# Kernel optimization log

Hardware: AMD Instinct MI355X
Metric: run time of the kernel (lower is better)

## Reference

```python
import jax, jax.numpy as jnp
import numpy as np

B, N, L, S = 32, 100000, 12, 256
SIGMA = 1.0          # gaussian filter sigma (pixels)
PIXEL = 1.0          # sampling rate (A/px)
LAMBDA = 0.0197      # electron wavelength at 300 kV (A)
CS = 2.7e7           # spherical aberration (A)
Q0 = 0.1             # amplitude contrast


def setup_inputs() -> dict:
    key = jax.random.key(0)
    ks = jax.random.split(key, 10)
    return {
        "c_nma": jax.random.normal(ks[0], (B, L), jnp.float32),
        "delta_euler": 0.1 * jax.random.normal(ks[1], (B, 3), jnp.float32),
        "delta_shifts": jax.random.normal(ks[2], (B, 2), jnp.float32),
        "coords": (jax.random.uniform(ks[3], (N, 3), jnp.float32) - 0.5) * (S / 2.0),
        "basis_x": 0.01 * jax.random.normal(ks[4], (N, L), jnp.float32),
        "basis_y": 0.01 * jax.random.normal(ks[5], (N, L), jnp.float32),
        "basis_z": 0.01 * jax.random.normal(ks[6], (N, L), jnp.float32),
        "euler_base": 2.0 * np.pi * jax.random.uniform(ks[7], (B, 3), jnp.float32),
        "shifts_base": 2.0 * jax.random.normal(ks[8], (B, 2), jnp.float32),
        "defocus": 1e4 + 1.5e4 * jax.random.uniform(ks[9], (B,), jnp.float32),
    }


def _euler_to_rot(eu):
    # ZYZ (xmipp) convention: rot, tilt, psi -> [B,3,3]
    rot, tilt, psi = eu[..., 0], eu[..., 1], eu[..., 2]
    ca, sa = jnp.cos(rot), jnp.sin(rot)
    cb, sb = jnp.cos(tilt), jnp.sin(tilt)
    cg, sg = jnp.cos(psi), jnp.sin(psi)
    r0 = jnp.stack([cg * cb * ca - sg * sa, cg * cb * sa + sg * ca, -cg * sb], -1)
    r1 = jnp.stack([-sg * cb * ca - cg * sa, -sg * cb * sa + cg * ca, sg * sb], -1)
    r2 = jnp.stack([sb * ca, sb * sa, cb], -1)
    return jnp.stack([r0, r1, r2], -2)


def _forward(c_nma, delta_euler, delta_shifts, coords, basis_x, basis_y, basis_z,
             euler_base, shifts_base, defocus):
    # deformation field + apply: [B,N]
    c_x = coords[:, 0][None, :] + jnp.einsum('bl,nl->bn', c_nma, basis_x)
    c_y = coords[:, 1][None, :] + jnp.einsum('bl,nl->bn', c_nma, basis_y)
    c_z = coords[:, 2][None, :] + jnp.einsum('bl,nl->bn', c_nma, basis_z)
    p = jnp.stack([c_x, c_y, c_z], -1)               # [B,N,3]

    # bond lengths between consecutive atoms: [B,N-1]
    dvec = p[:, 1:] - p[:, :-1]
    bondk = jnp.sqrt(jnp.sum(dvec * dvec, -1) + 1e-12)
    # angles at interior atoms: [B,N-2]
    u = p[:, :-2] - p[:, 1:-1]
    v = p[:, 2:] - p[:, 1:-1]
    cosang = jnp.sum(u * v, -1) / (
        jnp.sqrt(jnp.sum(u * u, -1)) * jnp.sqrt(jnp.sum(v * v, -1)) + 1e-12)
    anglek = jnp.arccos(jnp.clip(cosang, -0.9999, 0.9999))

    # alignment with refined euler angles, keep x/y projection rows: [B,N,2]
    R = _euler_to_rot(euler_base + delta_euler)
    proj = jnp.einsum('bij,bnj->bni', R[:, :2], p)
    sh = shifts_base + delta_shifts
    x = proj[..., 0] + sh[:, 0:1] + S / 2.0
    y = proj[..., 1] + sh[:, 1:2] + S / 2.0

    # bilinear scatter-add splat into [B,S,S]
    x = jnp.clip(x, 0.0, S - 1.001)
    y = jnp.clip(y, 0.0, S - 1.001)
    x0 = jnp.floor(x).astype(jnp.int32); fx = x - x0
    y0 = jnp.floor(y).astype(jnp.int32); fy = y - y0
    x1, y1 = x0 + 1, y0 + 1
    b_idx = jnp.arange(B, dtype=jnp.int32)[:, None]
    flat = lambda xi, yi: ((b_idx * S + yi) * S + xi).ravel()
    idx = jnp.concatenate([flat(x0, y0), flat(x1, y0), flat(x0, y1), flat(x1, y1)])
    w = jnp.concatenate([((1 - fx) * (1 - fy)).ravel(), (fx * (1 - fy)).ravel(),
                         ((1 - fx) * fy).ravel(), (fx * fy).ravel()])
    img = jnp.zeros(B * S * S, x.dtype).at[idx].add(w).reshape(B, S, S)

    # gaussian low-pass + CTF in Fourier space
    freq_y = jnp.fft.fftfreq(S).astype(x.dtype)
    freq_x = jnp.fft.rfftfreq(S).astype(x.dtype)
    s2 = freq_y[:, None] ** 2 + freq_x[None, :] ** 2          # [S, S//2+1]
    G = jnp.exp(-2.0 * (jnp.pi * SIGMA) ** 2 * s2)
    F = jnp.fft.rfft2(img) * G
    s2a = s2 / (PIXEL ** 2)
    chi = (jnp.pi * LAMBDA * defocus[:, None, None] * s2a
           - 0.5 * jnp.pi * CS * LAMBDA ** 3 * s2a ** 2)
    ctf = -(jnp.sqrt(1.0 - Q0 ** 2) * jnp.sin(chi) + Q0 * jnp.cos(chi))
    decoded = jnp.fft.irfft2(F * ctf, s=(S, S))
    return decoded, bondk, anglek


def reference(c_nma, delta_euler, delta_shifts, coords, basis_x, basis_y, basis_z,
              euler_base, shifts_base, defocus):
    return _forward(c_nma, delta_euler, delta_shifts, coords, basis_x, basis_y,
                    basis_z, euler_base, shifts_base, defocus)
```

## Files before the change

### kernel.cpp

```cpp
#include <hip/hip_runtime.h>
#include <math.h>

namespace {
constexpr int kB = 32;
constexpr int kN = 100000;
constexpr int kL = 12;
constexpr int kS = 256;
constexpr int kBG = 8;
constexpr int kWOwn = 62;
constexpr int kTile = 4 * kWOwn;
constexpr int kNB = (kN + kTile - 1) / kTile;
constexpr int kSlot = 64;
constexpr int kKx = 130;

constexpr float kGauss = (float)(2.0 * M_PI * M_PI);
constexpr float kA1 = (float)(M_PI * 0.0197);
constexpr float kA2 = (float)(0.5 * M_PI * 2.7e7 * 0.0197 * 0.0197 * 0.0197);
constexpr float kW1 = 0.99498743710661995f;
constexpr float kQ0 = 0.1f;
}

__device__ __forceinline__ void build_tw(float2* tw, int t) {
  if (t < 128) {
    float s, c;
    sincosf((float)M_PI / 128.0f * (float)t, &s, &c);
    tw[t] = make_float2(c, s);
  }
}

template <int SIGN>
__device__ __forceinline__ void fft256w(float2 v[4], float2* fb, int lane,
                                        const float2* tw) {
#pragma unroll
  for (int m = 1; m <= 64; m *= 4) {
    int l = lane & (m - 1);
    int jm = lane - l;
    float2 wv = tw[jm];
    float c = wv.x;
    float s = (SIGN < 0) ? -wv.y : wv.y;
    float2 A0 = v[0], A1 = v[1], A2 = v[2], A3 = v[3];
    float s02x = A0.x + A2.x, s02y = A0.y + A2.y;
    float d02x = A0.x - A2.x, d02y = A0.y - A2.y;
    float s13x = A1.x + A3.x, s13y = A1.y + A3.y;
    float d13x = A1.x - A3.x, d13y = A1.y - A3.y;
    float jdx = (SIGN < 0) ? d13y : -d13y;
    float jdy = (SIGN < 0) ? -d13x : d13x;
    float t1x = d02x + jdx, t1y = d02y + jdy;
    float t2x = s02x - s13x, t2y = s02y - s13y;
    float t3x = d02x - jdx, t3y = d02y - jdy;
    float c2 = c * c - s * s, s2 = 2.f * c * s;
    float c3 = c2 * c - s2 * s, s3 = c2 * s + s2 * c;
    int ob = 4 * jm + l;
    fb[ob]         = make_float2(s02x + s13x, s02y + s13y);
    fb[ob + m]     = make_float2(c * t1x - s * t1y, c * t1y + s * t1x);
    fb[ob + 2 * m] = make_float2(c2 * t2x - s2 * t2y, c2 * t2y + s2 * t2x);
    fb[ob + 3 * m] = make_float2(c3 * t3x - s3 * t3y, c3 * t3y + s3 * t3x);
    v[0] = fb[lane];
    v[1] = fb[lane + 64];
    v[2] = fb[lane + 128];
    v[3] = fb[lane + 192];
  }
}

__global__ __launch_bounds__(256) void k_deform(
    const float* __restrict__ c_nma, const float* __restrict__ delta_euler,
    const float* __restrict__ delta_shifts, const float* __restrict__ coords,
    const float* __restrict__ basis_x, const float* __restrict__ basis_y,
    const float* __restrict__ basis_z, const float* __restrict__ euler_base,
    const float* __restrict__ shifts_base,
    unsigned* __restrict__ xy_bkt, int* __restrict__ cnt,
    float* __restrict__ bond, float* __restrict__ angle) {
  __shared__ float cn_s[kBG][kL];
  __shared__ float rsh_s[kBG][8];
  __shared__ int bcnt[kBG][8];

  const int t = threadIdx.x;
  const int wave = t >> 6, lane = t & 63;
  const int bg = blockIdx.y * kBG;
  const int xb = blockIdx.x;
  const int n = xb * kTile + wave * kWOwn + lane;
  const bool owner = (lane < kWOwn) && (n < kN);
  const int nc = min(n, kN - 1);

  if (t < kBG * kL) cn_s[t / kL][t % kL] = c_nma[(bg + t / kL) * kL + (t % kL)];
  if (t < kBG) {
    int b = bg + t;
    float rot  = euler_base[b * 3 + 0] + delta_euler[b * 3 + 0];
    float tilt = euler_base[b * 3 + 1] + delta_euler[b * 3 + 1];
    float psi  = euler_base[b * 3 + 2] + delta_euler[b * 3 + 2];
    float ca = cosf(rot), sa = sinf(rot);
    float cb = cosf(tilt), sb = sinf(tilt);
    float cg = cosf(psi), sg = sinf(psi);
    rsh_s[t][0] = cg * cb * ca - sg * sa;
    rsh_s[t][1] = cg * cb * sa + sg * ca;
    rsh_s[t][2] = -cg * sb;
    rsh_s[t][3] = -sg * cb * ca - cg * sa;
    rsh_s[t][4] = -sg * cb * sa + cg * ca;
    rsh_s[t][5] = sg * sb;
    rsh_s[t][6] = shifts_base[b * 2 + 0] + delta_shifts[b * 2 + 0] + 128.0f;
    rsh_s[t][7] = shifts_base[b * 2 + 1] + delta_shifts[b * 2 + 1] + 128.0f;
  }
  if (t < kBG * 8) bcnt[t >> 3][t & 7] = 0;

  const float cx = coords[nc * 3 + 0];
  const float cy = coords[nc * 3 + 1];
  const float cz = coords[nc * 3 + 2];
  float bx[kL], by[kL], bz[kL];
  {
    const float4* px4 = reinterpret_cast<const float4*>(basis_x + (size_t)nc * kL);
    const float4* py4 = reinterpret_cast<const float4*>(basis_y + (size_t)nc * kL);
    const float4* pz4 = reinterpret_cast<const float4*>(basis_z + (size_t)nc * kL);
#pragma unroll
    for (int q = 0; q < 3; ++q) {
      float4 vx = px4[q], vy = py4[q], vz = pz4[q];
      bx[q * 4 + 0] = vx.x; bx[q * 4 + 1] = vx.y; bx[q * 4 + 2] = vx.z; bx[q * 4 + 3] = vx.w;
      by[q * 4 + 0] = vy.x; by[q * 4 + 1] = vy.y; by[q * 4 + 2] = vy.z; by[q * 4 + 3] = vy.w;
      bz[q * 4 + 0] = vz.x; bz[q * 4 + 1] = vz.y; bz[q * 4 + 2] = vz.z; bz[q * 4 + 3] = vz.w;
    }
  }
  __syncthreads();

#pragma unroll
  for (int bi = 0; bi < kBG; ++bi) {
    const int b = bg + bi;
    float px = cx, py = cy, pz = cz;
#pragma unroll
    for (int l = 0; l < kL; ++l) {
      float cc = cn_s[bi][l];
      px = fmaf(cc, bx[l], px);
      py = fmaf(cc, by[l], py);
      pz = fmaf(cc, bz[l], pz);
    }
    float p1x = __shfl_down(px, 1), p1y = __shfl_down(py, 1), p1z = __shfl_down(pz, 1);
    float dx = p1x - px, dy = p1y - py, dz = p1z - pz;
    float dd = fmaf(dx, dx, fmaf(dy, dy, dz * dz));
    float d1x = __shfl_down(dx, 1), d1y = __shfl_down(dy, 1), d1z = __shfl_down(dz, 1);

    if (owner) {
      float xr = fmaf(rsh_s[bi][0], px, fmaf(rsh_s[bi][1], py, fmaf(rsh_s[bi][2], pz, rsh_s[bi][6])));
      float yr = fmaf(rsh_s[bi][3], px, fmaf(rsh_s[bi][4], py, fmaf(rsh_s[bi][5], pz, rsh_s[bi][7])));
      xr = fminf(fmaxf(xr, 0.0f), 254.999f);
      yr = fminf(fmaxf(yr, 0.0f), 254.999f);
      unsigned xf = (unsigned)(xr * 256.0f);
      unsigned yf = (unsigned)(yr * 256.0f);
      unsigned u = (yf << 16) | xf;
      unsigned y0i = yf >> 8;
      unsigned band = y0i >> 5;
      int rank = atomicAdd(&bcnt[bi][band], 1);
      if (rank < kSlot)
        xy_bkt[(((size_t)b * 8 + band) * kNB + xb) * kSlot + rank] = u;
      if ((y0i & 31u) == 31u) {
        unsigned band1 = band + 1;
        int r2 = atomicAdd(&bcnt[bi][band1], 1);
        if (r2 < kSlot)
          xy_bkt[(((size_t)b * 8 + band1) * kNB + xb) * kSlot + r2] = u;
      }
      if (n < kN - 1) {
        __builtin_nontemporal_store(sqrtf(dd + 1e-12f),
                                    &bond[(size_t)b * (kN - 1) + n]);
      }
      if (n < kN - 2) {
        float vv = fmaf(d1x, d1x, fmaf(d1y, d1y, d1z * d1z));
        float uv = -fmaf(dx, d1x, fmaf(dy, d1y, dz * d1z));
        float cosang = uv * rsqrtf(dd * vv);
        cosang = fminf(fmaxf(cosang, -0.9999f), 0.9999f);
        float ax = fabsf(cosang);
        float rt = sqrtf(1.0f - ax);
        float pp = fmaf(fmaf(fmaf(-0.0187293f, ax, 0.0742610f), ax, -0.2121144f),
                        ax, 1.5707288f);
        float res = rt * pp;
        __builtin_nontemporal_store((cosang >= 0.f) ? res : (float)M_PI - res,
                                    &angle[(size_t)b * (kN - 2) + n]);
      }
    }
  }
  __syncthreads();
  if (t < kBG * 8) {
    int po = t >> 3, bandx = t & 7;
    cnt[((bg + po) * 8 + bandx) * kNB + xb] = min(bcnt[po][bandx], kSlot);
  }
}

__global__ __launch_bounds__(1024) void k_splat_fft(
    const unsigned* __restrict__ xy_bkt, const int* __restrict__ cnt,
    float2* __restrict__ FcT) {
  __shared__ unsigned tile[32 * 256];
  __shared__ float2 fbuf[16][256];
  __shared__ float2 tw[128];
  __shared__ int cnt_s[kNB];
  const int t = threadIdx.x;
  const int b = blockIdx.x >> 3;
  const int band = blockIdx.x & 7;
  const int r0 = band * 32;
  build_tw(tw, t);
  for (int i = t; i < 32 * 256; i += 1024) tile[i] = 0u;
  for (int i = t; i < kNB; i += 1024) cnt_s[i] = cnt[(b * 8 + band) * kNB + i];
  __syncthreads();

  const int w = t >> 6, lane = t & 63;
  const unsigned* segbase = xy_bkt + ((size_t)b * 8 + band) * kNB * kSlot;

  auto splat1 = [&](unsigned u) {
    int yf = (int)(u >> 16);
    int xf = (int)(u & 0xFFFFu);
    int ry = (yf >> 8) - r0;
    int x0 = xf >> 8;
    int fx = xf & 255, fy = yf & 255;
    int gx = 256 - fx, gy = 256 - fy;
    if ((unsigned)ry < 32u) {
      int base = ry * 256 + x0;
      atomicAdd(&tile[base],     (unsigned)((gx * gy + 2) >> 2));
      atomicAdd(&tile[base + 1], (unsigned)((fx * gy + 2) >> 2));
    }
    if ((unsigned)(ry + 1) < 32u) {
      int base = (ry + 1) * 256 + x0;
      atomicAdd(&tile[base],     (unsigned)((gx * fy + 2) >> 2));
      atomicAdd(&tile[base + 1], (unsigned)((fx * fy + 2) >> 2));
    }
  };

  for (int j = w; j < kNB; j += 16) {
    int cc = cnt_s[j];
    if (lane < cc) splat1(segbase[(size_t)j * kSlot + lane]);
  }
  __syncthreads();

  const int rowA = 2 * w;
  constexpr float scale = 1.0f / 16384.0f;
  float2 v[4];
#pragma unroll
  for (int j = 0; j < 4; ++j) {
    int i = lane + 64 * j;
    v[j] = make_float2((float)tile[rowA * 256 + i] * scale,
                       (float)tile[(rowA + 1) * 256 + i] * scale);
  }
  fft256w<-1>(v, fbuf[w], lane, tw);
  float2* a = fbuf[w];
  const int y = r0 + rowA;
#pragma unroll
  for (int j = 0; j < 2; ++j) {
    int k = lane + 64 * j;
    float2 Zk = a[k], Zm = a[(256 - k) & 255];
    float4 o = make_float4(0.5f * (Zk.x + Zm.x), 0.5f * (Zk.y - Zm.y),
                           0.5f * (Zk.y + Zm.y), 0.5f * (Zm.x - Zk.x));
    *reinterpret_cast<float4*>(&FcT[((size_t)b * kKx + k) * kS + y]) = o;
  }
  if (lane == 0) {
    float2 Zk = a[128];
    *reinterpret_cast<float4*>(&FcT[((size_t)b * kKx + 128) * kS + y]) =
        make_float4(Zk.x, 0.f, Zk.y, 0.f);
  }
}

__global__ __launch_bounds__(256) void k_fft_cols(float2* __restrict__ FcT,
                                                  const float* __restrict__ defocus) {
  __shared__ float2 fbuf[4][256];
  __shared__ float2 tw[128];
  const int t = threadIdx.x, w = t >> 6, lane = t & 63;
  build_tw(tw, t);
  const int b = blockIdx.x / 33;
  const int kx = (blockIdx.x % 33) * 4 + w;
  __syncthreads();
  if (kx > 128) return;
  float2* col = FcT + ((size_t)b * kKx + kx) * kS;
  float2 v[4];
#pragma unroll
  for (int j = 0; j < 4; ++j) v[j] = col[lane + 64 * j];
  fft256w<-1>(v, fbuf[w], lane, tw);

  const float D = defocus[b];
  const float fxv = (float)kx * (1.0f / 256.0f);
  const float fx2 = fxv * fxv;
#pragma unroll
  for (int j = 0; j < 4; ++j) {
    int ky = lane + 64 * j;
    float fyv = (float)(ky < 128 ? ky : ky - 256) * (1.0f / 256.0f);
    float s2 = fyv * fyv + fx2;
    float G = __expf(-kGauss * s2);
    float chi = kA1 * D * s2 - kA2 * s2 * s2;
    float sn, cn;
    sincosf(chi, &sn, &cn);
    float H = G * (-(kW1 * sn + kQ0 * cn));
    v[j].x *= H;
    v[j].y *= H;
  }
  fft256w<1>(v, fbuf[w], lane, tw);
#pragma unroll
  for (int j = 0; j < 4; ++j) col[lane + 64 * j] = v[j];
}

__global__ __launch_bounds__(256) void k_fft_rows_inv(const float2* __restrict__ FcT,
                                                      float* __restrict__ out) {
  __shared__ float2 fbuf[4][256];
  __shared__ float4 smT[4][132];
  __shared__ float2 tw[128];
  const int t = threadIdx.x, w = t >> 6, lane = t & 63;
  build_tw(tw, t);
  const int b = blockIdx.x >> 5;
  const int pp = (blockIdx.x & 31) * 4 + w;
  const int y = 2 * pp;

  const float4* Fp = reinterpret_cast<const float4*>(FcT + (size_t)b * kKx * kS + y);
  const size_t kstep = kS / 2;
  smT[w][lane]      = Fp[(size_t)lane * kstep];
  smT[w][lane + 64] = Fp[(size_t)(lane + 64) * kstep];
  if (lane == 0) smT[w][128] = Fp[(size_t)128 * kstep];
  __syncthreads();

  float2 v[4];
  {
    float4 f = smT[w][lane];
    v[0] = make_float2(f.x - f.w, f.y + f.z);
  }
  {
    float4 f = smT[w][lane + 64];
    v[1] = make_float2(f.x - f.w, f.y + f.z);
  }
  if (lane == 0) {
    float4 f = smT[w][128];
    v[2] = make_float2(f.x - f.w, f.y + f.z);
  } else {
    float4 f = smT[w][128 - lane];
    v[2] = make_float2(f.x + f.w, -f.y + f.z);
  }
  {
    float4 f = smT[w][64 - lane];
    v[3] = make_float2(f.x + f.w, -f.y + f.z);
  }
  fft256w<1>(v, fbuf[w], lane, tw);

  float* o0 = out + ((size_t)b * kS + y) * kS;
  float* o1 = o0 + kS;
#pragma unroll
  for (int j = 0; j < 4; ++j) {
    int i = lane + 64 * j;
    o0[i] = v[j].x * (1.0f / 65536.0f);
    o1[i] = v[j].y * (1.0f / 65536.0f);
  }
}

extern "C" void kernel_launch(void* const* d_in, const int* in_sizes, int n_in,
                              void* d_out, int out_size, void* d_ws, size_t ws_size,
                              hipStream_t stream) {
  const float* c_nma        = (const float*)d_in[0];
  const float* delta_euler  = (const float*)d_in[1];
  const float* delta_shifts = (const float*)d_in[2];
  const float* coords       = (const float*)d_in[3];
  const float* basis_x      = (const float*)d_in[4];
  const float* basis_y      = (const float*)d_in[5];
  const float* basis_z      = (const float*)d_in[6];
  const float* euler_base   = (const float*)d_in[7];
  const float* shifts_base  = (const float*)d_in[8];
  const float* defocus      = (const float*)d_in[9];

  float* out = (float*)d_out;
  float* decoded = out;
  float* bond    = out + (size_t)kB * kS * kS;
  float* angle   = bond + (size_t)kB * (kN - 1);

  char* ws = (char*)d_ws;
  const size_t bktBytes = (size_t)kB * 8 * kNB * kSlot * sizeof(unsigned);
  unsigned* xy_bkt = (unsigned*)ws;
  int*      cnt    = (int*)(ws + bktBytes);
  float2*   FcT    = (float2*)(ws + (size_t)28 * 1024 * 1024);

  dim3 gd(kNB, kB / kBG);
  k_deform<<<gd, 256, 0, stream>>>(c_nma, delta_euler, delta_shifts, coords,
                                   basis_x, basis_y, basis_z, euler_base,
                                   shifts_base, xy_bkt, cnt, bond, angle);
  k_splat_fft<<<kB * 8, 1024, 0, stream>>>(xy_bkt, cnt, FcT);
  k_fft_cols<<<kB * 33, 256, 0, stream>>>(FcT, defocus);
  k_fft_rows_inv<<<kB * 32, 256, 0, stream>>>(FcT, decoded);
}
```

Before: 57.09 us.

## Fuse splat, column FFT and inverse row FFT into one cooperative kernel

Merges the three post-deform kernels into a single cooperative launch of 256 blocks of 1024 threads, with grid-wide syncs between the splat/row-FFT, column-FFT+CTF, and inverse row-FFT phases. Shared memory is reused: the splat tile aliases the transpose staging buffer. The aim is to drop two kernel launch gaps and the tail drain between them. In exchange it depends on all 256 large blocks being co-resident, adds grid-sync cost, and runs the column and inverse phases with the smaller fixed grid.

```diff
diff --git a/kernel.cpp b/kernel.cpp
--- a/kernel.cpp
+++ b/kernel.cpp
@@ -1,5 +1,8 @@
 #include <hip/hip_runtime.h>
+#include <hip/hip_cooperative_groups.h>
 #include <math.h>
+
+namespace cg = cooperative_groups;
 
 namespace {
 constexpr int kB = 32;
@@ -181,161 +184,156 @@
   }
 }
 
-__global__ __launch_bounds__(1024) void k_splat_fft(
+__global__ __launch_bounds__(1024) void k_fft_all(
     const unsigned* __restrict__ xy_bkt, const int* __restrict__ cnt,
-    float2* __restrict__ FcT) {
-  __shared__ unsigned tile[32 * 256];
+    float2* __restrict__ FcT, const float* __restrict__ defocus,
+    float* __restrict__ out) {
+  __shared__ float4 big[16][132];
   __shared__ float2 fbuf[16][256];
   __shared__ float2 tw[128];
   __shared__ int cnt_s[kNB];
+  unsigned* tile = reinterpret_cast<unsigned*>(&big[0][0]);
+
   const int t = threadIdx.x;
-  const int b = blockIdx.x >> 3;
-  const int band = blockIdx.x & 7;
-  const int r0 = band * 32;
+  const int w = t >> 6, lane = t & 63;
+  const int bid = blockIdx.x;
   build_tw(tw, t);
-  for (int i = t; i < 32 * 256; i += 1024) tile[i] = 0u;
-  for (int i = t; i < kNB; i += 1024) cnt_s[i] = cnt[(b * 8 + band) * kNB + i];
-  __syncthreads();
-
-  const int w = t >> 6, lane = t & 63;
-  const unsigned* segbase = xy_bkt + ((size_t)b * 8 + band) * kNB * kSlot;
-
-  auto splat1 = [&](unsigned u) {
-    int yf = (int)(u >> 16);
-    int xf = (int)(u & 0xFFFFu);
-    int ry = (yf >> 8) - r0;
-    int x0 = xf >> 8;
-    int fx = xf & 255, fy = yf & 255;
-    int gx = 256 - fx, gy = 256 - fy;
-    if ((unsigned)ry < 32u) {
-      int base = ry * 256 + x0;
-      atomicAdd(&tile[base],     (unsigned)((gx * gy + 2) >> 2));
-      atomicAdd(&tile[base + 1], (unsigned)((fx * gy + 2) >> 2));
-    }
-    if ((unsigned)(ry + 1) < 32u) {
-      int base = (ry + 1) * 256 + x0;
-      atomicAdd(&tile[base],     (unsigned)((gx * fy + 2) >> 2));
-      atomicAdd(&tile[base + 1], (unsigned)((fx * fy + 2) >> 2));
-    }
-  };
-
-  for (int j = w; j < kNB; j += 16) {
-    int cc = cnt_s[j];
-    if (lane < cc) splat1(segbase[(size_t)j * kSlot + lane]);
-  }
-  __syncthreads();
-
-  const int rowA = 2 * w;
-  constexpr float scale = 1.0f / 16384.0f;
-  float2 v[4];
-#pragma unroll
-  for (int j = 0; j < 4; ++j) {
-    int i = lane + 64 * j;
-    v[j] = make_float2((float)tile[rowA * 256 + i] * scale,
-                       (float)tile[(rowA + 1) * 256 + i] * scale);
-  }
-  fft256w<-1>(v, fbuf[w], lane, tw);
-  float2* a = fbuf[w];
-  const int y = r0 + rowA;
-#pragma unroll
-  for (int j = 0; j < 2; ++j) {
-    int k = lane + 64 * j;
-    float2 Zk = a[k], Zm = a[(256 - k) & 255];
-    float4 o = make_float4(0.5f * (Zk.x + Zm.x), 0.5f * (Zk.y - Zm.y),
-                           0.5f * (Zk.y + Zm.y), 0.5f * (Zm.x - Zk.x));
-    *reinterpret_cast<float4*>(&FcT[((size_t)b * kKx + k) * kS + y]) = o;
-  }
-  if (lane == 0) {
-    float2 Zk = a[128];
-    *reinterpret_cast<float4*>(&FcT[((size_t)b * kKx + 128) * kS + y]) =
-        make_float4(Zk.x, 0.f, Zk.y, 0.f);
-  }
-}
-
-__global__ __launch_bounds__(256) void k_fft_cols(float2* __restrict__ FcT,
-                                                  const float* __restrict__ defocus) {
-  __shared__ float2 fbuf[4][256];
-  __shared__ float2 tw[128];
-  const int t = threadIdx.x, w = t >> 6, lane = t & 63;
-  build_tw(tw, t);
-  const int b = blockIdx.x / 33;
-  const int kx = (blockIdx.x % 33) * 4 + w;
-  __syncthreads();
-  if (kx > 128) return;
-  float2* col = FcT + ((size_t)b * kKx + kx) * kS;
-  float2 v[4];
-#pragma unroll
-  for (int j = 0; j < 4; ++j) v[j] = col[lane + 64 * j];
-  fft256w<-1>(v, fbuf[w], lane, tw);
-
-  const float D = defocus[b];
-  const float fxv = (float)kx * (1.0f / 256.0f);
-  const float fx2 = fxv * fxv;
-#pragma unroll
-  for (int j = 0; j < 4; ++j) {
-    int ky = lane + 64 * j;
-    float fyv = (float)(ky < 128 ? ky : ky - 256) * (1.0f / 256.0f);
-    float s2 = fyv * fyv + fx2;
-    float G = __expf(-kGauss * s2);
-    float chi = kA1 * D * s2 - kA2 * s2 * s2;
-    float sn, cn;
-    sincosf(chi, &sn, &cn);
-    float H = G * (-(kW1 * sn + kQ0 * cn));
-    v[j].x *= H;
-    v[j].y *= H;
-  }
-  fft256w<1>(v, fbuf[w], lane, tw);
-#pragma unroll
-  for (int j = 0; j < 4; ++j) col[lane + 64 * j] = v[j];
-}
-
-__global__ __launch_bounds__(256) void k_fft_rows_inv(const float2* __restrict__ FcT,
-                                                      float* __restrict__ out) {
-  __shared__ float2 fbuf[4][256];
-  __shared__ float4 smT[4][132];
-  __shared__ float2 tw[128];
-  const int t = threadIdx.x, w = t >> 6, lane = t & 63;
-  build_tw(tw, t);
-  const int b = blockIdx.x >> 5;
-  const int pp = (blockIdx.x & 31) * 4 + w;
-  const int y = 2 * pp;
-
-  const float4* Fp = reinterpret_cast<const float4*>(FcT + (size_t)b * kKx * kS + y);
-  const size_t kstep = kS / 2;
-  smT[w][lane]      = Fp[(size_t)lane * kstep];
-  smT[w][lane + 64] = Fp[(size_t)(lane + 64) * kstep];
-  if (lane == 0) smT[w][128] = Fp[(size_t)128 * kstep];
-  __syncthreads();
-
-  float2 v[4];
+  cg::grid_group grid = cg::this_grid();
+
   {
-    float4 f = smT[w][lane];
-    v[0] = make_float2(f.x - f.w, f.y + f.z);
-  }
+    const int b = bid >> 3, band = bid & 7, r0 = band * 32;
+    for (int i = t; i < 32 * 256; i += 1024) tile[i] = 0u;
+    for (int i = t; i < kNB; i += 1024) cnt_s[i] = cnt[(b * 8 + band) * kNB + i];
+    __syncthreads();
+
+    const unsigned* segbase = xy_bkt + ((size_t)b * 8 + band) * kNB * kSlot;
+    auto splat1 = [&](unsigned u) {
+      int yf = (int)(u >> 16);
+      int xf = (int)(u & 0xFFFFu);
+      int ry = (yf >> 8) - r0;
+      int x0 = xf >> 8;
+      int fx = xf & 255, fy = yf & 255;
+      int gx = 256 - fx, gy = 256 - fy;
+      if ((unsigned)ry < 32u) {
+        int base = ry * 256 + x0;
+        atomicAdd(&tile[base],     (unsigned)((gx * gy + 2) >> 2));
+        atomicAdd(&tile[base + 1], (unsigned)((fx * gy + 2) >> 2));
+      }
+      if ((unsigned)(ry + 1) < 32u) {
+        int base = (ry + 1) * 256 + x0;
+        atomicAdd(&tile[base],     (unsigned)((gx * fy + 2) >> 2));
+        atomicAdd(&tile[base + 1], (unsigned)((fx * fy + 2) >> 2));
+      }
+    };
+    for (int j = w; j < kNB; j += 16) {
+      int cc = cnt_s[j];
+      if (lane < cc) splat1(segbase[(size_t)j * kSlot + lane]);
+    }
+    __syncthreads();
+
+    const int rowA = 2 * w;
+    constexpr float scale = 1.0f / 16384.0f;
+    float2 v[4];
+#pragma unroll
+    for (int j = 0; j < 4; ++j) {
+      int i = lane + 64 * j;
+      v[j] = make_float2((float)tile[rowA * 256 + i] * scale,
+                         (float)tile[(rowA + 1) * 256 + i] * scale);
+    }
+    fft256w<-1>(v, fbuf[w], lane, tw);
+    float2* a = fbuf[w];
+    const int y = r0 + rowA;
+#pragma unroll
+    for (int j = 0; j < 2; ++j) {
+      int k = lane + 64 * j;
+      float2 Zk = a[k], Zm = a[(256 - k) & 255];
+      float4 o = make_float4(0.5f * (Zk.x + Zm.x), 0.5f * (Zk.y - Zm.y),
+                             0.5f * (Zk.y + Zm.y), 0.5f * (Zm.x - Zk.x));
+      *reinterpret_cast<float4*>(&FcT[((size_t)b * kKx + k) * kS + y]) = o;
+    }
+    if (lane == 0) {
+      float2 Zk = a[128];
+      *reinterpret_cast<float4*>(&FcT[((size_t)b * kKx + 128) * kS + y]) =
+          make_float4(Zk.x, 0.f, Zk.y, 0.f);
+    }
+  }
+  grid.sync();
+
   {
-    float4 f = smT[w][lane + 64];
-    v[1] = make_float2(f.x - f.w, f.y + f.z);
-  }
-  if (lane == 0) {
-    float4 f = smT[w][128];
-    v[2] = make_float2(f.x - f.w, f.y + f.z);
-  } else {
-    float4 f = smT[w][128 - lane];
-    v[2] = make_float2(f.x + f.w, -f.y + f.z);
-  }
+    const int gw = bid * 16 + w;
+    for (int task = gw; task < kB * 129; task += 4096) {
+      int b = task / 129, kx = task - b * 129;
+      float2* col = FcT + ((size_t)b * kKx + kx) * kS;
+      float2 v[4];
+#pragma unroll
+      for (int j = 0; j < 4; ++j) v[j] = col[lane + 64 * j];
+      fft256w<-1>(v, fbuf[w], lane, tw);
+      const float D = defocus[b];
+      const float fxv = (float)kx * (1.0f / 256.0f);
+      const float fx2 = fxv * fxv;
+#pragma unroll
+      for (int j = 0; j < 4; ++j) {
+        int ky = lane + 64 * j;
+        float fyv = (float)(ky < 128 ? ky : ky - 256) * (1.0f / 256.0f);
+        float s2 = fyv * fyv + fx2;
+        float G = __expf(-kGauss * s2);
+        float chi = kA1 * D * s2 - kA2 * s2 * s2;
+        float sn, cn;
+        sincosf(chi, &sn, &cn);
+        float H = G * (-(kW1 * sn + kQ0 * cn));
+        v[j].x *= H;
+        v[j].y *= H;
+      }
+      fft256w<1>(v, fbuf[w], lane, tw);
+#pragma unroll
+      for (int j = 0; j < 4; ++j) col[lane + 64 * j] = v[j];
+    }
+  }
+  grid.sync();
+
   {
-    float4 f = smT[w][64 - lane];
-    v[3] = make_float2(f.x + f.w, -f.y + f.z);
-  }
-  fft256w<1>(v, fbuf[w], lane, tw);
-
-  float* o0 = out + ((size_t)b * kS + y) * kS;
-  float* o1 = o0 + kS;
-#pragma unroll
-  for (int j = 0; j < 4; ++j) {
-    int i = lane + 64 * j;
-    o0[i] = v[j].x * (1.0f / 65536.0f);
-    o1[i] = v[j].y * (1.0f / 65536.0f);
+    const int gw = bid * 16 + w;
+    const int b = gw >> 7, pp = gw & 127;
+    const int y = 2 * pp;
+    float4* smT = &big[w][0];
+
+    const float4* Fp =
+        reinterpret_cast<const float4*>(FcT + (size_t)b * kKx * kS + y);
+    const size_t kstep = kS / 2;
+    smT[lane]      = Fp[(size_t)lane * kstep];
+    smT[lane + 64] = Fp[(size_t)(lane + 64) * kstep];
+    if (lane == 0) smT[128] = Fp[(size_t)128 * kstep];
+
+    float2 v[4];
+    {
+      float4 f = smT[lane];
+      v[0] = make_float2(f.x - f.w, f.y + f.z);
+    }
+    {
+      float4 f = smT[lane + 64];
+      v[1] = make_float2(f.x - f.w, f.y + f.z);
+    }
+    if (lane == 0) {
+      float4 f = smT[128];
+      v[2] = make_float2(f.x - f.w, f.y + f.z);
+    } else {
+      float4 f = smT[128 - lane];
+      v[2] = make_float2(f.x + f.w, -f.y + f.z);
+    }
+    {
+      float4 f = smT[64 - lane];
+      v[3] = make_float2(f.x + f.w, -f.y + f.z);
+    }
+    fft256w<1>(v, fbuf[w], lane, tw);
+
+    float* o0 = out + ((size_t)b * kS + y) * kS;
+    float* o1 = o0 + kS;
+#pragma unroll
+    for (int j = 0; j < 4; ++j) {
+      int i = lane + 64 * j;
+      o0[i] = v[j].x * (1.0f / 65536.0f);
+      o1[i] = v[j].y * (1.0f / 65536.0f);
+    }
   }
 }
 
@@ -368,7 +366,9 @@
   k_deform<<<gd, 256, 0, stream>>>(c_nma, delta_euler, delta_shifts, coords,
                                    basis_x, basis_y, basis_z, euler_base,
                                    shifts_base, xy_bkt, cnt, bond, angle);
-  k_splat_fft<<<kB * 8, 1024, 0, stream>>>(xy_bkt, cnt, FcT);
-  k_fft_cols<<<kB * 33, 256, 0, stream>>>(FcT, defocus);
-  k_fft_rows_inv<<<kB * 32, 256, 0, stream>>>(FcT, decoded);
-}
+
+  void* args[] = {(void*)&xy_bkt, (void*)&cnt, (void*)&FcT,
+                  (void*)&defocus, (void*)&decoded};
+  hipLaunchCooperativeKernel((const void*)k_fft_all, dim3(256), dim3(1024),
+                             args, 0, stream);
+}
```

After: 136.6 us. 2.39x slower.
